# Performance work log

Hardware: AMD Instinct MI355X
Metric: run time of the kernel (lower is better)

Reference implementation:

```python
import jax, jax.numpy as jnp
import numpy as np

LINE_W = 30.0   # pos_weight for confidence BCE
GAMMA = 2.0     # focal loss gamma
PULL = 0.5      # pull margin
PUSH = 1.0      # push margin
CONF_W, OFF_W, EMB_W, EMBID_W, CLS_W = 1.0, 0.5, 1.0, 1.0, 1.0
NC = 8          # num_classes
EPS = 1e-5
DICE_W = 5.0


def _dice(p, g, m):
    # masked dice terms for one sample; p,g,m: [HW] (m is 0/1 float)
    spg = (p * g * m).sum(); spp = (p * p * m).sum(); sgg = (g * g * m).sum()
    q = 1.0 - p; h = 1.0 - g
    s2pg = (q * h * m).sum(); s2pp = (q * q * m).sum(); s2gg = (h * h * m).sum()
    t = (1.0 - (spg + EPS) / (spp + sgg + EPS)) - (s2pg + EPS) / (s2pp + s2gg + EPS)
    return jnp.where(m.sum() > 0, t, 0.0)


def _emb(p, g, m):
    # pull/push loss for one sample; p: [HW] float, g: [HW] int ids, m: [HW] bool
    pair = m[:, None] & m[None, :]
    same = pair & (g[:, None] == g[None, :])   # includes diagonal, matches gt_square==1
    diff = pair & (g[:, None] != g[None, :])
    d = jnp.abs(p[:, None] - p[None, :])        # 1-channel norm == abs
    cs = same.sum(); cd = diff.sum()
    pull = (jnp.maximum(d - PULL, 0.0) * same).sum() / jnp.maximum(cs, 1).astype(p.dtype)
    push = jnp.where(cd > 0,
                     (jnp.maximum(PUSH - d, 0.0) * diff).sum() / jnp.maximum(cd, 1).astype(p.dtype),
                     0.0)
    return pull + push


def _total(outputs, gt_conf, gt_ox, gt_oy, gt_cls, line_idx, ign, fg, line_id):
    B = outputs.shape[0]
    x = outputs[:, 0:1]                 # confidence logits
    pred_off = outputs[:, 1:3]
    pred_emb = outputs[:, 3].reshape(B, -1)
    pred_emb_id = outputs[:, 4].reshape(B, -1)
    cls_logit = outputs[:, 5:5 + NC]
    f32 = outputs.dtype
    ign_m = (ign > 0).astype(f32)
    fg_f = (fg > 0).astype(f32)
    fg_b = (fg.reshape(B, -1) > 0)

    # focal BCE-with-logits (pos_weight on positive term)
    ls = jax.nn.log_sigmoid(x); lns = jax.nn.log_sigmoid(-x)
    bce = -(gt_conf * ls + (1.0 - gt_conf) * lns)
    p = jnp.exp(-bce)
    conf = -(LINE_W * gt_conf * ls + (1.0 - gt_conf) * lns)
    focal = (1.0 - p) ** GAMMA * conf
    conf_loss = (focal * ign_m).sum() / jnp.maximum(ign_m.sum(), 1.0)

    # dice (per sample on ignore-masked pixels)
    p_sig = jax.nn.sigmoid(x).reshape(B, -1)
    dice = jax.vmap(_dice)(p_sig, gt_conf.reshape(B, -1), ign_m.reshape(B, -1)).sum()
    conf_loss = conf_loss + DICE_W * dice / B

    # masked MSE on sigmoid(offset)
    gt_off = jnp.concatenate([gt_ox, gt_oy], 1)
    se = (jax.nn.sigmoid(pred_off) - gt_off) ** 2
    off_loss = (se * fg_f).sum() / jnp.maximum(2.0 * fg_f.sum(), 1.0)

    # pull/push embedding losses
    emb_loss = jax.vmap(_emb)(pred_emb, line_idx.reshape(B, -1), fg_b).sum() / B
    emb_id_loss = jax.vmap(_emb)(pred_emb_id, line_id.reshape(B, -1), fg_b).sum() / B

    # masked BCE on sigmoid(cls)
    lsc = jax.nn.log_sigmoid(cls_logit); lnsc = jax.nn.log_sigmoid(-cls_logit)
    bce_c = -(gt_cls * lsc + (1.0 - gt_cls) * lnsc)
    cls_loss = (bce_c * fg_f).sum() / jnp.maximum(NC * fg_f.sum(), 1.0)

    return (CONF_W * conf_loss + OFF_W * off_loss + EMB_W * emb_loss
            + EMBID_W * emb_id_loss + CLS_W * cls_loss)


def setup_inputs() -> dict:
    key = jax.random.key(0)
    ks = jax.random.split(key, 10)
    B, H, W = 4, 64, 64
    C = 5 + NC
    f32 = jnp.float32
    return {
        'outputs': jax.random.normal(ks[0], (B, C, H, W), f32),
        'batch_gt_confidence': jax.random.uniform(ks[1], (B, 1, H, W), f32),
        'batch_gt_offset_x': jax.random.uniform(ks[2], (B, 1, H, W), f32),
        'batch_gt_offset_y': jax.random.uniform(ks[3], (B, 1, H, W), f32),
        'batch_gt_line_index': jax.random.randint(ks[4], (B, 1, H, W), 0, 8, jnp.int32),
        'batch_ignore_mask': jax.random.randint(ks[5], (B, 1, H, W), 0, 2, jnp.int32),
        'batch_foreground_mask': jax.random.randint(ks[6], (B, 1, H, W), 0, 2, jnp.int32),
        'batch_gt_line_id': jax.random.randint(ks[7], (B, 1, H, W), 0, 8, jnp.int32),
        'batch_gt_line_cls': jax.random.bernoulli(ks[8], 0.5, (B, NC, H, W)).astype(f32),
        'batch_foreground_expand_mask': jax.random.randint(ks[9], (B, 1, H, W), 0, 2, jnp.int32),
    }


def reference(outputs, batch_gt_confidence, batch_gt_offset_x, batch_gt_offset_y,
              batch_gt_line_index, batch_ignore_mask, batch_foreground_mask,
              batch_gt_line_id, batch_gt_line_cls, batch_foreground_expand_mask):
    # batch_foreground_expand_mask is unused by the original forward's math.
    return _total(outputs, batch_gt_confidence, batch_gt_offset_x, batch_gt_offset_y,
                  batch_gt_line_cls, batch_gt_line_index, batch_ignore_mask,
                  batch_foreground_mask, batch_gt_line_id)
```

## Files before the change

### kernel.cpp

```cpp
#include <hip/hip_runtime.h>

constexpr int B = 4, N = 4096;
constexpr int CCH = 13;
constexpr float LINE_W = 30.0f;
constexpr double EPS = 1e-05;
constexpr double DICE_W = 5.0;
constexpr int BCAP = 1024;
constexpr int PUSHB = 512;
constexpr int NPAIRB = PUSHB + 256;

constexpr int EWP_OFF   = 0;
constexpr int PA_OFF    = 2816;
constexpr int BP_OFF    = 3328;
constexpr int CURS_OFF  = 3840;
constexpr int VCURS_OFF = 3904;
constexpr int BUCK_OFF  = 4096;
constexpr int VC_OFF    = BUCK_OFF + 64 * BCAP;

__device__ inline float logsig(float x) {
    return fminf(x, 0.f) - log1pf(expf(-fabsf(x)));
}
__device__ inline float wave_reduce(float v) {
    #pragma unroll
    for (int off = 32; off > 0; off >>= 1) v += __shfl_down(v, off, 64);
    return v;
}
__device__ inline double wave_reduce_d(double v) {
    #pragma unroll
    for (int off = 32; off > 0; off >>= 1) v += __shfl_down(v, off, 64);
    return v;
}
__device__ inline float rdlane(float v, int k) {
    return __uint_as_float(__builtin_amdgcn_readlane(__float_as_uint(v), k));
}

__global__ __launch_bounds__(1024) void prep_kernel(
        const float* __restrict__ outs, const float* __restrict__ gconf,
        const float* __restrict__ gox,  const float* __restrict__ goy,
        const int*   __restrict__ lidx, const int*   __restrict__ ign,
        const int*   __restrict__ fg,   const int*   __restrict__ lid,
        const float* __restrict__ gcls, float* __restrict__ ws) {
    const int tid = threadIdx.x, ln = tid & 63;

    if (blockIdx.x < 8) {
        const int eb = blockIdx.x, e = eb >> 2, b = eb & 3;
        const int* gsrc = e ? lid : lidx;
        const float* pch = outs + ((size_t)b * CCH + 3 + e) * N;

        __shared__ int lcurs[9];
        if (tid < 9) lcurs[tid] = 0;
        __syncthreads();

        #pragma unroll
        for (int it = 0; it < 4; ++it) {
            const int n = it * 1024 + tid;
            const bool v = fg[b * N + n] > 0;
            const float val = pch[n];
            const int cc = gsrc[b * N + n] & 7;
            const unsigned long long below = (1ull << ln) - 1ull;
            const unsigned long long vm = __ballot(v);

            int mycnt = 0;
            int myrank = 0;
            #pragma unroll
            for (int c = 0; c < 8; ++c) {
                const unsigned long long m = __ballot(v && cc == c);
                const int cnt = __popcll(m);
                if (ln == c) mycnt = cnt;
                if (cc == c) myrank = __popcll(m & below);
            }
            if (ln == 8) mycnt = __popcll(vm);
            const int myvrank = __popcll(vm & below);

            int abase = 0;
            if (ln < 9) abase = atomicAdd(&lcurs[ln], mycnt);
            const int cbase = __shfl(abase, cc, 64);
            const int vbase = __shfl(abase, 8, 64);

            if (v) {
                ws[VC_OFF + eb * 4096 + vbase + myvrank] = val;
                const int slot = cbase + myrank;
                if (slot < BCAP) ws[BUCK_OFF + (eb * 8 + cc) * BCAP + slot] = val;
            }
        }
        __syncthreads();

        int* curs  = (int*)(ws + CURS_OFF);
        int* vcurs = (int*)(ws + VCURS_OFF);
        const float QNAN = __int_as_float(0x7FC00000);
        if (tid < 8) curs[eb * 8 + tid] = min(lcurs[tid], BCAP);
        if (tid == 8) vcurs[eb] = lcurs[8];
        #pragma unroll
        for (int c = 0; c < 8; ++c) {
            const int mm = min(lcurs[c], BCAP);
            const int pad = ((mm + 255) & ~255) - mm;
            if (tid < pad) ws[BUCK_OFF + (eb * 8 + c) * BCAP + mm + tid] = QNAN;
        }
        const int mv = lcurs[8];
        const int padv = ((mv + 255) & ~255) - mv;
        if (tid < padv && mv + tid < 4096) ws[VC_OFF + eb * 4096 + mv + tid] = QNAN;
    } else {
        const int idx = (blockIdx.x - 8) * 1024 + tid;
        const int b = idx >> 12, n = idx & 4095;
        const int pix = idx;
        const int pslot = idx >> 6;
        const float* ob = outs + (size_t)b * CCH * N;

        const float x  = ob[n];
        const float g  = gconf[pix];
        const float im = ign[pix] > 0 ? 1.f : 0.f;
        const float ff = fg[pix] > 0 ? 1.f : 0.f;

        const float ls  = logsig(x);
        const float lns = logsig(-x);
        const float bce = -(g * ls + (1.f - g) * lns);
        const float p   = expf(-bce);
        const float conf = -(LINE_W * g * ls + (1.f - g) * lns);
        const float om  = 1.f - p;
        const float focal = om * om * conf * im;

        const float ps = 1.f / (1.f + expf(-x));
        const float q = 1.f - ps, hh = 1.f - g;
        const float spg = ps * g * im,  spp = ps * ps * im,  sgg = g * g * im;
        const float s2pg = q * hh * im, s2pp = q * q * im,   s2gg = hh * hh * im;

        const float sox = 1.f / (1.f + expf(-ob[1 * N + n]));
        const float soy = 1.f / (1.f + expf(-ob[2 * N + n]));
        const float dx = sox - gox[pix], dy = soy - goy[pix];
        const float se = (dx * dx + dy * dy) * ff;

        float cl = 0.f;
        #pragma unroll
        for (int c = 0; c < 8; ++c) {
            const float z  = ob[(5 + c) * N + n];
            const float gc = gcls[((size_t)b * 8 + c) * N + n];
            cl += -(gc * logsig(z) + (1.f - gc) * logsig(-z));
        }
        cl *= ff;

        float vals[11] = {spg, spp, sgg, s2pg, s2pp, s2gg, im, focal, se, ff, cl};
        #pragma unroll
        for (int qq = 0; qq < 11; ++qq) {
            const float r = wave_reduce(vals[qq]);
            if (ln == 0) ws[EWP_OFF + qq * 256 + pslot] = r;
        }
    }
}

__global__ __launch_bounds__(256) void pair_kernel(float* __restrict__ ws) {
    const int bx  = blockIdx.x;
    const int tid = threadIdx.x;
    const int ln  = tid & 63;
    const int wv  = tid >> 6;
    const int* curs  = (const int*)(ws + CURS_OFF);
    const int* vcurs = (const int*)(ws + VCURS_OFF);

    float a0 = 0.f, a1 = 0.f, a2 = 0.f, a3 = 0.f;

    if (bx < PUSHB) {
        const int eb = bx >> 6, it = (bx >> 2) & 15, js = bx & 3;
        const int m = min(vcurs[eb], 4096);
        if (it * 256 < m) {
            const float* arr = ws + VC_OFF + eb * 4096;
            const float pi = arr[it * 256 + tid];
            const int nch = (m + 63) >> 6;
            for (int cj = js; cj < nch; cj += 4) {
                const float jv = arr[cj * 64 + ln];
                #pragma unroll
                for (int k = 0; k < 64; k += 2) {
                    const float s0 = rdlane(jv, k);
                    const float s1 = rdlane(jv, k + 1);
                    a0 += fmaxf(1.f - fabsf(pi - s0), 0.f);
                    a2 += fmaxf(1.f - fabsf(pi - s1), 0.f);
                }
            }
        }
    } else {
        const int bx2 = bx - PUSHB;
        const int bk = bx2 >> 2, js = bx2 & 3;
        const int m = min(curs[bk], BCAP);
        const float* arr = ws + BUCK_OFF + bk * BCAP;
        const int nch = (m + 63) >> 6;
        for (int i0 = 0; i0 < m; i0 += 256) {
            const float pi = arr[i0 + tid];
            for (int cj = js; cj < nch; cj += 4) {
                const float jv = arr[cj * 64 + ln];
                #pragma unroll
                for (int k = 0; k < 64; k += 2) {
                    const float d0 = fabsf(pi - rdlane(jv, k));
                    const float d1 = fabsf(pi - rdlane(jv, k + 1));
                    a0 += fmaxf(d0 - 0.5f, 0.f);
                    a2 += fmaxf(d1 - 0.5f, 0.f);
                    a1 += fmaxf(1.f - d0, 0.f);
                    a3 += fmaxf(1.f - d1, 0.f);
                }
            }
        }
    }

    __shared__ float red[4][2];
    const float r0 = wave_reduce(a0 + a2);
    const float r1 = wave_reduce(a1 + a3);
    if (ln == 0) { red[wv][0] = r0; red[wv][1] = r1; }
    __syncthreads();
    if (tid == 0) {
        const float s0 = red[0][0] + red[1][0] + red[2][0] + red[3][0];
        const float s1 = red[0][1] + red[1][1] + red[2][1] + red[3][1];
        if (bx < PUSHB) {
            ws[PA_OFF + bx] = s0;
        } else {
            ws[BP_OFF + (bx - PUSHB) * 2 + 0] = s0;
            ws[BP_OFF + (bx - PUSHB) * 2 + 1] = s1;
        }
    }
}

__global__ __launch_bounds__(256) void finalize_kernel(
        const float* __restrict__ ws, float* __restrict__ out) {
    const int tid = threadIdx.x, ln = tid & 63, wv = tid >> 6;
    __shared__ double ewb[4][7];
    __shared__ double gsum[4];
    __shared__ double pa[8];
    __shared__ double bp[8][2];
    __shared__ double sred[4];

    #pragma unroll
    for (int q = 0; q < 7; ++q) {
        double v = (double)ws[EWP_OFF + q * 256 + tid];
        v = wave_reduce_d(v);
        if (ln == 0) ewb[wv][q] = v;
    }
    for (int q = 7; q < 11; ++q) {
        double v = (double)ws[EWP_OFF + q * 256 + tid];
        v = wave_reduce_d(v);
        if (ln == 0) sred[wv] = v;
        __syncthreads();
        if (tid == 0) gsum[q - 7] = sred[0] + sred[1] + sred[2] + sred[3];
        __syncthreads();
    }
    #pragma unroll
    for (int q = 0; q < 2; ++q) {
        const int eb = wv * 2 + q;
        double v = (double)ws[PA_OFF + eb * 64 + ln];
        v = wave_reduce_d(v);
        if (ln == 0) pa[eb] = v;
    }
    #pragma unroll
    for (int q = 0; q < 2; ++q) {
        double v = (double)ws[BP_OFF + tid * 2 + q];
        #pragma unroll
        for (int off = 16; off > 0; off >>= 1) v += __shfl_down(v, off, 32);
        if ((tid & 31) == 0) bp[tid >> 5][q] = v;
    }
    __syncthreads();
    if (tid != 0) return;

    const int* curs = (const int*)(ws + CURS_OFF);

    double ign_sum = 0.0, dice = 0.0;
    for (int b = 0; b < B; ++b) {
        const double msum = ewb[b][6];
        ign_sum += msum;
        const double t = 1.0 - (ewb[b][0] + EPS) / (ewb[b][1] + ewb[b][2] + EPS)
                             - (ewb[b][3] + EPS) / (ewb[b][4] + ewb[b][5] + EPS);
        dice += (msum > 0.0) ? t : 0.0;
    }
    const double focal = gsum[0], se = gsum[1], ffs = gsum[2], clsum = gsum[3];
    const double conf_loss = focal / fmax(ign_sum, 1.0) + DICE_W * dice / B;
    const double off_loss  = se / fmax(2.0 * ffs, 1.0);

    double embv[2] = {0.0, 0.0};
    for (int e = 0; e < 2; ++e)
        for (int b = 0; b < B; ++b) {
            const int eb = e * 4 + b;
            double cs = 0.0, nv = 0.0;
            for (int c = 0; c < 8; ++c) {
                const double x = (double)curs[eb * 8 + c];
                cs += x * x; nv += x;
            }
            const double cd = nv * nv - cs;
            const double pull = bp[eb][0] / fmax(cs, 1.0);
            const double pushsum = pa[eb] - bp[eb][1];
            const double push = (cd > 0.0) ? pushsum / fmax(cd, 1.0) : 0.0;
            embv[e] += pull + push;
        }

    const double cls_loss = clsum / fmax(8.0 * ffs, 1.0);
    const double total = conf_loss + 0.5 * off_loss
                       + embv[0] / B + embv[1] / B + cls_loss;
    out[0] = (float)total;
}

extern "C" void kernel_launch(void* const* d_in, const int* in_sizes, int n_in,
                              void* d_out, int out_size, void* d_ws, size_t ws_size,
                              hipStream_t stream) {
    const float* outs  = (const float*)d_in[0];
    const float* gconf = (const float*)d_in[1];
    const float* gox   = (const float*)d_in[2];
    const float* goy   = (const float*)d_in[3];
    const int*   lidx  = (const int*)d_in[4];
    const int*   ign   = (const int*)d_in[5];
    const int*   fg    = (const int*)d_in[6];
    const int*   lid   = (const int*)d_in[7];
    const float* gcls  = (const float*)d_in[8];
    float* ws = (float*)d_ws;

    prep_kernel<<<24, 1024, 0, stream>>>(outs, gconf, gox, goy, lidx, ign, fg, lid, gcls, ws);
    pair_kernel<<<NPAIRB, 256, 0, stream>>>(ws);
    finalize_kernel<<<1, 256, 0, stream>>>(ws, (float*)d_out);
}
```

Before: 39.68 us.

## Fuse compaction and pairwise loss into one kernel using shared-memory compaction

Merges the prep and pair kernels into a single launch. Each pair block now compacts its own masked embedding values into shared memory with a ballot plus prefix-scan, so the global-memory bucket and valid-value buffers and one kernel boundary are no longer needed. The work split also changes: each push block handles all rows of a sample with a strided column slice, and each bucket block processes a whole class bucket with no BCAP cap. Every pair block now redundantly reads the 4096-element inputs, and bucket blocks with large classes may become long single-block tails.

```diff
diff --git a/kernel.cpp b/kernel.cpp
--- a/kernel.cpp
+++ b/kernel.cpp
@@ -5,17 +5,17 @@
 constexpr float LINE_W = 30.0f;
 constexpr double EPS = 1e-05;
 constexpr double DICE_W = 5.0;
-constexpr int BCAP = 1024;
-constexpr int PUSHB = 512;
-constexpr int NPAIRB = PUSHB + 256;
-
-constexpr int EWP_OFF   = 0;
-constexpr int PA_OFF    = 2816;
-constexpr int BP_OFF    = 3328;
-constexpr int CURS_OFF  = 3840;
-constexpr int VCURS_OFF = 3904;
-constexpr int BUCK_OFF  = 4096;
-constexpr int VC_OFF    = BUCK_OFF + 64 * BCAP;
+
+constexpr int PUSH_SL = 32;
+constexpr int PUSHB = 8 * PUSH_SL;
+constexpr int BUCKB = 64;
+constexpr int ELEMB = 64;
+constexpr int NB = PUSHB + BUCKB + ELEMB;
+
+constexpr int EWP_OFF  = 0;
+constexpr int PA_OFF   = 2816;
+constexpr int BP_OFF   = 3072;
+constexpr int CURS_OFF = 3200;
 
 __device__ inline float logsig(float x) {
     return fminf(x, 0.f) - log1pf(expf(-fabsf(x)));
@@ -34,73 +34,125 @@
     return __uint_as_float(__builtin_amdgcn_readlane(__float_as_uint(v), k));
 }
 
-__global__ __launch_bounds__(1024) void prep_kernel(
+__global__ __launch_bounds__(256) void fused_kernel(
         const float* __restrict__ outs, const float* __restrict__ gconf,
         const float* __restrict__ gox,  const float* __restrict__ goy,
         const int*   __restrict__ lidx, const int*   __restrict__ ign,
         const int*   __restrict__ fg,   const int*   __restrict__ lid,
         const float* __restrict__ gcls, float* __restrict__ ws) {
-    const int tid = threadIdx.x, ln = tid & 63;
-
-    if (blockIdx.x < 8) {
-        const int eb = blockIdx.x, e = eb >> 2, b = eb & 3;
-        const int* gsrc = e ? lid : lidx;
+    const int bx = blockIdx.x, tid = threadIdx.x;
+    const int ln = tid & 63, wv = tid >> 6;
+
+    __shared__ float sv[4096];
+    __shared__ unsigned long long smask[16][4];
+    __shared__ int scnt[64];
+    __shared__ int sbase[64];
+    __shared__ int stot;
+    __shared__ float red[4][2];
+
+    if (bx < PUSHB + BUCKB) {
+        const bool isPush = bx < PUSHB;
+        const int eb  = isPush ? (bx >> 5) : ((bx - PUSHB) >> 3);
+        const int cls = isPush ? -1 : ((bx - PUSHB) & 7);
+        const int js  = isPush ? (bx & 31) : 0;
+        const int e = eb >> 2, b = eb & 3;
         const float* pch = outs + ((size_t)b * CCH + 3 + e) * N;
-
-        __shared__ int lcurs[9];
-        if (tid < 9) lcurs[tid] = 0;
-        __syncthreads();
-
-        #pragma unroll
-        for (int it = 0; it < 4; ++it) {
-            const int n = it * 1024 + tid;
-            const bool v = fg[b * N + n] > 0;
-            const float val = pch[n];
-            const int cc = gsrc[b * N + n] & 7;
-            const unsigned long long below = (1ull << ln) - 1ull;
-            const unsigned long long vm = __ballot(v);
-
-            int mycnt = 0;
-            int myrank = 0;
+        const int* fgp = fg + b * N;
+        const int* gp  = (e ? lid : lidx) + b * N;
+
+        unsigned pred = 0;
+        float vals[16];
+        #pragma unroll
+        for (int ch = 0; ch < 16; ++ch) {
+            const int n = ch * 256 + tid;
+            bool v = fgp[n] > 0;
+            if (!isPush) v = v && ((gp[n] & 7) == cls);
+            vals[ch] = pch[n];
+            const unsigned long long mk = __ballot(v);
+            pred |= (v ? 1u : 0u) << ch;
+            if (ln == 0) { smask[ch][wv] = mk; scnt[ch * 4 + wv] = __popcll(mk); }
+        }
+        __syncthreads();
+
+        if (tid < 64) {
+            const int c = scnt[tid];
+            int inc = c;
             #pragma unroll
-            for (int c = 0; c < 8; ++c) {
-                const unsigned long long m = __ballot(v && cc == c);
-                const int cnt = __popcll(m);
-                if (ln == c) mycnt = cnt;
-                if (cc == c) myrank = __popcll(m & below);
-            }
-            if (ln == 8) mycnt = __popcll(vm);
-            const int myvrank = __popcll(vm & below);
-
-            int abase = 0;
-            if (ln < 9) abase = atomicAdd(&lcurs[ln], mycnt);
-            const int cbase = __shfl(abase, cc, 64);
-            const int vbase = __shfl(abase, 8, 64);
-
-            if (v) {
-                ws[VC_OFF + eb * 4096 + vbase + myvrank] = val;
-                const int slot = cbase + myrank;
-                if (slot < BCAP) ws[BUCK_OFF + (eb * 8 + cc) * BCAP + slot] = val;
-            }
-        }
-        __syncthreads();
-
-        int* curs  = (int*)(ws + CURS_OFF);
-        int* vcurs = (int*)(ws + VCURS_OFF);
-        const float QNAN = __int_as_float(0x7FC00000);
-        if (tid < 8) curs[eb * 8 + tid] = min(lcurs[tid], BCAP);
-        if (tid == 8) vcurs[eb] = lcurs[8];
-        #pragma unroll
-        for (int c = 0; c < 8; ++c) {
-            const int mm = min(lcurs[c], BCAP);
-            const int pad = ((mm + 255) & ~255) - mm;
-            if (tid < pad) ws[BUCK_OFF + (eb * 8 + c) * BCAP + mm + tid] = QNAN;
-        }
-        const int mv = lcurs[8];
-        const int padv = ((mv + 255) & ~255) - mv;
-        if (tid < padv && mv + tid < 4096) ws[VC_OFF + eb * 4096 + mv + tid] = QNAN;
+            for (int off = 1; off < 64; off <<= 1) {
+                const int t = __shfl_up(inc, off, 64);
+                if (ln >= off) inc += t;
+            }
+            sbase[tid] = inc - c;
+            if (tid == 63) stot = inc;
+        }
+        __syncthreads();
+        const int m = min(stot, 4096);
+
+        #pragma unroll
+        for (int ch = 0; ch < 16; ++ch) {
+            if ((pred >> ch) & 1u) {
+                const unsigned long long mk = smask[ch][wv];
+                const int slot = sbase[ch * 4 + wv] + __popcll(mk & ((1ull << ln) - 1ull));
+                if (slot < 4096) sv[slot] = vals[ch];
+            }
+        }
+        const int mpad = (m + 255) & ~255;
+        for (int i = m + tid; i < mpad; i += 256) sv[i] = __int_as_float(0x7FC00000);
+        __syncthreads();
+
+        float a0 = 0.f, a1 = 0.f, a2 = 0.f, a3 = 0.f;
+        const int nch = (m + 63) >> 6;
+        if (isPush) {
+            for (int i0 = 0; i0 < m; i0 += 256) {
+                const float pi = sv[i0 + tid];
+                for (int cj = js; cj < nch; cj += PUSH_SL) {
+                    const float jv = sv[cj * 64 + ln];
+                    #pragma unroll
+                    for (int k = 0; k < 64; k += 2) {
+                        const float s0 = rdlane(jv, k);
+                        const float s1 = rdlane(jv, k + 1);
+                        a0 += fmaxf(1.f - fabsf(pi - s0), 0.f);
+                        a2 += fmaxf(1.f - fabsf(pi - s1), 0.f);
+                    }
+                }
+            }
+        } else {
+            for (int i0 = 0; i0 < m; i0 += 256) {
+                const float pi = sv[i0 + tid];
+                for (int cj = 0; cj < nch; ++cj) {
+                    const float jv = sv[cj * 64 + ln];
+                    #pragma unroll
+                    for (int k = 0; k < 64; k += 2) {
+                        const float d0 = fabsf(pi - rdlane(jv, k));
+                        const float d1 = fabsf(pi - rdlane(jv, k + 1));
+                        a0 += fmaxf(d0 - 0.5f, 0.f);
+                        a2 += fmaxf(d1 - 0.5f, 0.f);
+                        a1 += fmaxf(1.f - d0, 0.f);
+                        a3 += fmaxf(1.f - d1, 0.f);
+                    }
+                }
+            }
+        }
+
+        const float r0 = wave_reduce(a0 + a2);
+        const float r1 = wave_reduce(a1 + a3);
+        if (ln == 0) { red[wv][0] = r0; red[wv][1] = r1; }
+        __syncthreads();
+        if (tid == 0) {
+            const float s0 = red[0][0] + red[1][0] + red[2][0] + red[3][0];
+            const float s1 = red[0][1] + red[1][1] + red[2][1] + red[3][1];
+            if (isPush) {
+                ws[PA_OFF + bx] = s0;
+            } else {
+                const int bk = bx - PUSHB;
+                ws[BP_OFF + bk * 2 + 0] = s0;
+                ws[BP_OFF + bk * 2 + 1] = s1;
+                ((int*)(ws + CURS_OFF))[bk] = m;
+            }
+        }
     } else {
-        const int idx = (blockIdx.x - 8) * 1024 + tid;
+        const int blk = bx - (PUSHB + BUCKB);
+        const int idx = blk * 256 + tid;
         const int b = idx >> 12, n = idx & 4095;
         const int pix = idx;
         const int pslot = idx >> 6;
@@ -143,74 +195,6 @@
         for (int qq = 0; qq < 11; ++qq) {
             const float r = wave_reduce(vals[qq]);
             if (ln == 0) ws[EWP_OFF + qq * 256 + pslot] = r;
-        }
-    }
-}
-
-__global__ __launch_bounds__(256) void pair_kernel(float* __restrict__ ws) {
-    const int bx  = blockIdx.x;
-    const int tid = threadIdx.x;
-    const int ln  = tid & 63;
-    const int wv  = tid >> 6;
-    const int* curs  = (const int*)(ws + CURS_OFF);
-    const int* vcurs = (const int*)(ws + VCURS_OFF);
-
-    float a0 = 0.f, a1 = 0.f, a2 = 0.f, a3 = 0.f;
-
-    if (bx < PUSHB) {
-        const int eb = bx >> 6, it = (bx >> 2) & 15, js = bx & 3;
-        const int m = min(vcurs[eb], 4096);
-        if (it * 256 < m) {
-            const float* arr = ws + VC_OFF + eb * 4096;
-            const float pi = arr[it * 256 + tid];
-            const int nch = (m + 63) >> 6;
-            for (int cj = js; cj < nch; cj += 4) {
-                const float jv = arr[cj * 64 + ln];
-                #pragma unroll
-                for (int k = 0; k < 64; k += 2) {
-                    const float s0 = rdlane(jv, k);
-                    const float s1 = rdlane(jv, k + 1);
-                    a0 += fmaxf(1.f - fabsf(pi - s0), 0.f);
-                    a2 += fmaxf(1.f - fabsf(pi - s1), 0.f);
-                }
-            }
-        }
-    } else {
-        const int bx2 = bx - PUSHB;
-        const int bk = bx2 >> 2, js = bx2 & 3;
-        const int m = min(curs[bk], BCAP);
-        const float* arr = ws + BUCK_OFF + bk * BCAP;
-        const int nch = (m + 63) >> 6;
-        for (int i0 = 0; i0 < m; i0 += 256) {
-            const float pi = arr[i0 + tid];
-            for (int cj = js; cj < nch; cj += 4) {
-                const float jv = arr[cj * 64 + ln];
-                #pragma unroll
-                for (int k = 0; k < 64; k += 2) {
-                    const float d0 = fabsf(pi - rdlane(jv, k));
-                    const float d1 = fabsf(pi - rdlane(jv, k + 1));
-                    a0 += fmaxf(d0 - 0.5f, 0.f);
-                    a2 += fmaxf(d1 - 0.5f, 0.f);
-                    a1 += fmaxf(1.f - d0, 0.f);
-                    a3 += fmaxf(1.f - d1, 0.f);
-                }
-            }
-        }
-    }
-
-    __shared__ float red[4][2];
-    const float r0 = wave_reduce(a0 + a2);
-    const float r1 = wave_reduce(a1 + a3);
-    if (ln == 0) { red[wv][0] = r0; red[wv][1] = r1; }
-    __syncthreads();
-    if (tid == 0) {
-        const float s0 = red[0][0] + red[1][0] + red[2][0] + red[3][0];
-        const float s1 = red[0][1] + red[1][1] + red[2][1] + red[3][1];
-        if (bx < PUSHB) {
-            ws[PA_OFF + bx] = s0;
-        } else {
-            ws[BP_OFF + (bx - PUSHB) * 2 + 0] = s0;
-            ws[BP_OFF + (bx - PUSHB) * 2 + 1] = s1;
         }
     }
 }
@@ -238,19 +222,21 @@
         if (tid == 0) gsum[q - 7] = sred[0] + sred[1] + sred[2] + sred[3];
         __syncthreads();
     }
-    #pragma unroll
-    for (int q = 0; q < 2; ++q) {
-        const int eb = wv * 2 + q;
-        double v = (double)ws[PA_OFF + eb * 64 + ln];
-        v = wave_reduce_d(v);
-        if (ln == 0) pa[eb] = v;
-    }
-    #pragma unroll
-    for (int q = 0; q < 2; ++q) {
-        double v = (double)ws[BP_OFF + tid * 2 + q];
+    {
+        double v = (double)ws[PA_OFF + tid];
         #pragma unroll
         for (int off = 16; off > 0; off >>= 1) v += __shfl_down(v, off, 32);
-        if ((tid & 31) == 0) bp[tid >> 5][q] = v;
+        if ((tid & 31) == 0) pa[tid >> 5] = v;
+    }
+    if (tid < 64) {
+        double v0 = (double)ws[BP_OFF + tid * 2 + 0];
+        double v1 = (double)ws[BP_OFF + tid * 2 + 1];
+        #pragma unroll
+        for (int off = 4; off > 0; off >>= 1) {
+            v0 += __shfl_down(v0, off, 8);
+            v1 += __shfl_down(v1, off, 8);
+        }
+        if ((tid & 7) == 0) { bp[tid >> 3][0] = v0; bp[tid >> 3][1] = v1; }
     }
     __syncthreads();
     if (tid != 0) return;
@@ -305,7 +291,6 @@
     const float* gcls  = (const float*)d_in[8];
     float* ws = (float*)d_ws;
 
-    prep_kernel<<<24, 1024, 0, stream>>>(outs, gconf, gox, goy, lidx, ign, fg, lid, gcls, ws);
-    pair_kernel<<<NPAIRB, 256, 0, stream>>>(ws);
+    fused_kernel<<<NB, 256, 0, stream>>>(outs, gconf, gox, goy, lidx, ign, fg, lid, gcls, ws);
     finalize_kernel<<<1, 256, 0, stream>>>(ws, (float*)d_out);
 }
```

New measurement: 33.72 us, median of 2. -15.0%, faster.
